# Kernel optimization log

Measured on AMD Instinct MI355X. Metric: run time of the kernel, lower is better.

## Reference

```python
import jax, jax.numpy as jnp
import numpy as np

FEAT_DIM = 2048
HIDDEN = 1024
ATTN_DIM = 512
BATCH = 128
NPOS = 196


def setup_inputs() -> dict:
    key = jax.random.key(0)
    ks = jax.random.split(key, 8)
    # Linear layers use kaiming-uniform-ish init; plain scaled normal is fine for a numeric baseline.
    def lin(k, fan_in, fan_out):
        k1, k2 = jax.random.split(k)
        bound = 1.0 / np.sqrt(fan_in)
        W = jax.random.uniform(k1, (fan_out, fan_in), jnp.float32, -bound, bound)
        b = jax.random.uniform(k2, (fan_out,), jnp.float32, -bound, bound)
        return W, b
    We, be = lin(ks[0], FEAT_DIM, ATTN_DIM)
    Wd, bd = lin(ks[1], HIDDEN, ATTN_DIM)
    Wf, bf = lin(ks[2], ATTN_DIM, 1)
    encoder_out = jax.random.normal(ks[3], (BATCH, NPOS, FEAT_DIM), jnp.float32)
    hidden = jax.random.normal(ks[4], (BATCH, HIDDEN), jnp.float32)
    return {
        "encoder_out": encoder_out,
        "hidden": hidden,
        "We": We, "be": be,
        "Wd": Wd, "bd": bd,
        "Wf": Wf, "bf": bf,
    }


def reference(encoder_out, hidden, We, be, Wd, bd, Wf, bf):
    # enc: [B, P, A]; dec: [B, 1, A]
    enc = jnp.einsum('bpf,af->bpa', encoder_out, We) + be
    dec = (jnp.einsum('bh,ah->ba', hidden, Wd) + bd)[:, None, :]
    scores = jnp.tanh(enc + dec)
    # full_attn: [A] -> scalar per position; Wf has shape [1, A]
    scores = jnp.einsum('bpa,a->bp', scores, Wf[0]) + bf[0]
    alpha = jax.nn.softmax(scores, axis=1)  # [B, P]
    context = jnp.einsum('bpf,bp->bf', encoder_out, alpha)  # [B, F]
    return context, alpha
```

## Files before the change

### kernel.cpp

```cpp
#include <hip/hip_runtime.h>
#include <hip/hip_bf16.h>

typedef __bf16 bf16x8 __attribute__((ext_vector_type(8)));
typedef __bf16 bf16x4 __attribute__((ext_vector_type(4)));
typedef float f32x4 __attribute__((ext_vector_type(4)));

#define FEAT 2048
#define HID  1024
#define AD   512
#define NB   128
#define NP   196
#define MROWS (NB * NP)
#define BM 128
#define BN 128
#define BK 64
#define NSTEP (FEAT / BK)
#define NBLK (MROWS / BM * 4)

__global__ __launch_bounds__(256) void pack_we_k(const float* __restrict__ We,
                                                 __bf16* __restrict__ Bp) {
    int t = blockIdx.x * 256 + threadIdx.x;
    int a  = t >> 8;
    int f0 = (t & 255) << 3;
    const float4* src = reinterpret_cast<const float4*>(We + ((size_t)a << 11) + f0);
    float4 x0 = src[0], x1 = src[1];
    int nt = a >> 4, r = a & 15;
    int kt = f0 >> 5, g = (f0 >> 3) & 3;
    size_t off = (((size_t)(kt * 32 + nt) * 64) + (r + (g << 4))) << 3;
    union { __bf16 h[8]; bf16x8 v; } u;
    u.h[0] = (__bf16)x0.x; u.h[1] = (__bf16)x0.y; u.h[2] = (__bf16)x0.z; u.h[3] = (__bf16)x0.w;
    u.h[4] = (__bf16)x1.x; u.h[5] = (__bf16)x1.y; u.h[6] = (__bf16)x1.z; u.h[7] = (__bf16)x1.w;
    *reinterpret_cast<bf16x8*>(Bp + off) = u.v;
}

__global__ __launch_bounds__(256) void dec_k(const float* __restrict__ hidden,
                                             const float* __restrict__ Wd,
                                             const float* __restrict__ bd,
                                             const float* __restrict__ be,
                                             float* __restrict__ decb) {
    __shared__ float w[8][1028];
    const int tid = threadIdx.x;
    const int n0 = blockIdx.x << 3;
    const float4* wsrc = reinterpret_cast<const float4*>(Wd + ((size_t)n0 << 10));
    #pragma unroll
    for (int i = 0; i < 8; ++i)
        *reinterpret_cast<float4*>(&w[i][tid << 2]) = wsrc[(i << 8) + tid];
    __syncthreads();
    const int nl = tid & 7, b0 = tid >> 3;
    float acc[4] = {0.f, 0.f, 0.f, 0.f};
    const float4* wp = reinterpret_cast<const float4*>(&w[nl][0]);
    #pragma unroll 2
    for (int k4 = 0; k4 < 256; ++k4) {
        float4 wv = wp[k4];
        #pragma unroll
        for (int i = 0; i < 4; ++i) {
            const float4 h = reinterpret_cast<const float4*>(
                hidden + ((size_t)(b0 + (i << 5)) << 10))[k4];
            acc[i] = fmaf(wv.x, h.x, acc[i]);
            acc[i] = fmaf(wv.y, h.y, acc[i]);
            acc[i] = fmaf(wv.z, h.z, acc[i]);
            acc[i] = fmaf(wv.w, h.w, acc[i]);
        }
    }
    const float bias = bd[n0 + nl] + be[n0 + nl];
    #pragma unroll
    for (int i = 0; i < 4; ++i)
        decb[(size_t)(b0 + (i << 5)) * AD + n0 + nl] = acc[i] + bias;
}

__global__ __launch_bounds__(256, 3) void enc_score_k(
        const float* __restrict__ X, const __bf16* __restrict__ Bp,
        const float* __restrict__ decb, const float* __restrict__ Wf,
        float* __restrict__ spart) {
    __shared__ char Asm[2][BM * BK * 2];
    __shared__ float swave[2][BM];
    const int tid  = threadIdx.x;
    const int wave = tid >> 6, lane = tid & 63;
    const int lr = lane & 15, lg = lane >> 4;
    const int wm = wave >> 1, wn = wave & 1;
    const int vbid = (blockIdx.x & 7) * 98 + (blockIdx.x >> 3);
    const int rt = vbid >> 2, nq = vbid & 3;
    const int row0 = rt * BM;
    const int ncol0 = nq * BN + wn * 64;

    f32x4 acc[4][4];
    #pragma unroll
    for (int mt = 0; mt < 4; ++mt) {
        #pragma unroll
        for (int j = 0; j < 4; ++j) {
            const int row = wm * 64 + mt * 16 + lg * 4 + j;
            const int b = (unsigned)(row0 + row) / 196u;
            const float* dp = decb + (size_t)b * AD + ncol0 + lr;
            #pragma unroll
            for (int nt = 0; nt < 4; ++nt) acc[mt][nt][j] = dp[nt * 16];
        }
    }

    const int srow = tid >> 4;
    const int schk = tid & 15;
    const float* gA = X + (size_t)(row0 + srow) * FEAT + schk * 4;
    const int rswz = (lr & 7) << 4;
    const __bf16* Bq = Bp + ((size_t)(nq * 8 + wn * 4) << 9) + (lane << 3);

    float4 rA[8];
    #pragma unroll
    for (int i = 0; i < 8; ++i)
        rA[i] = *reinterpret_cast<const float4*>(gA + (size_t)(i * 16) * FEAT);
    #pragma unroll
    for (int i = 0; i < 8; ++i) {
        const int r = srow + 16 * i;
        union { __bf16 h[4]; bf16x4 v; } p;
        p.h[0] = (__bf16)rA[i].x; p.h[1] = (__bf16)rA[i].y;
        p.h[2] = (__bf16)rA[i].z; p.h[3] = (__bf16)rA[i].w;
        *reinterpret_cast<bf16x4*>(Asm[0] + r * 128 + ((schk * 8) ^ ((r & 7) << 4))) = p.v;
    }
    __syncthreads();

    int cur = 0;
    for (int t = 0; t < NSTEP; ++t) {
        bf16x8 bfr[8];
        {
            const __bf16* bs = Bq + (size_t)t * 32768;
            #pragma unroll
            for (int kt2 = 0; kt2 < 2; ++kt2)
                #pragma unroll
                for (int j = 0; j < 4; ++j)
                    bfr[kt2 * 4 + j] = *reinterpret_cast<const bf16x8*>(
                        bs + kt2 * 16384 + j * 512);
        }
        __builtin_amdgcn_sched_barrier(0);
        if (t + 1 < NSTEP) {
            const float* g = gA + (size_t)(t + 1) * BK;
            #pragma unroll
            for (int i = 0; i < 8; ++i)
                rA[i] = *reinterpret_cast<const float4*>(g + (size_t)(i * 16) * FEAT);
        }
        __builtin_amdgcn_sched_barrier(0);
        #pragma unroll
        for (int kt2 = 0; kt2 < 2; ++kt2) {
            #pragma unroll
            for (int mt = 0; mt < 4; ++mt) {
                const int R = wm * 64 + mt * 16 + lr;
                bf16x8 a = *reinterpret_cast<const bf16x8*>(
                    Asm[cur] + R * 128 + ((kt2 * 64 + lg * 16) ^ rswz));
                acc[mt][0] = __builtin_amdgcn_mfma_f32_16x16x32_bf16(a, bfr[kt2*4+0], acc[mt][0], 0, 0, 0);
                acc[mt][1] = __builtin_amdgcn_mfma_f32_16x16x32_bf16(a, bfr[kt2*4+1], acc[mt][1], 0, 0, 0);
                acc[mt][2] = __builtin_amdgcn_mfma_f32_16x16x32_bf16(a, bfr[kt2*4+2], acc[mt][2], 0, 0, 0);
                acc[mt][3] = __builtin_amdgcn_mfma_f32_16x16x32_bf16(a, bfr[kt2*4+3], acc[mt][3], 0, 0, 0);
            }
        }
        if (t + 1 < NSTEP) {
            #pragma unroll
            for (int i = 0; i < 8; ++i) {
                const int r = srow + 16 * i;
                union { __bf16 h[4]; bf16x4 v; } p;
                p.h[0] = (__bf16)rA[i].x; p.h[1] = (__bf16)rA[i].y;
                p.h[2] = (__bf16)rA[i].z; p.h[3] = (__bf16)rA[i].w;
                *reinterpret_cast<bf16x4*>(
                    Asm[cur ^ 1] + r * 128 + ((schk * 8) ^ ((r & 7) << 4))) = p.v;
            }
        }
        __syncthreads();
        cur ^= 1;
    }

    float wf[4];
    #pragma unroll
    for (int nt = 0; nt < 4; ++nt) wf[nt] = Wf[ncol0 + nt * 16 + lr];
    #pragma unroll
    for (int mt = 0; mt < 4; ++mt) {
        #pragma unroll
        for (int j = 0; j < 4; ++j) {
            float s = 0.f;
            #pragma unroll
            for (int nt = 0; nt < 4; ++nt) {
                float x = acc[mt][nt][j];
                float e = __expf(2.0f * x);
                float t = 1.0f - 2.0f / (e + 1.0f);
                s = fmaf(t, wf[nt], s);
            }
            s += __shfl_xor(s, 1); s += __shfl_xor(s, 2);
            s += __shfl_xor(s, 4); s += __shfl_xor(s, 8);
            if (lr == 0) swave[wn][wm * 64 + mt * 16 + lg * 4 + j] = s;
        }
    }
    __syncthreads();
    if (tid < BM)
        spart[(size_t)nq * MROWS + row0 + tid] = swave[0][tid] + swave[1][tid];
}

__global__ __launch_bounds__(64) void softmax_k(const float* __restrict__ spart,
                                                float* __restrict__ alpha) {
    const int b = blockIdx.x, lane = threadIdx.x;
    float v[4], e[4];
    float m = -3.0e38f;
    #pragma unroll
    for (int i = 0; i < 4; ++i) {
        int p = i * 64 + lane;
        if (p < NP) {
            int idx = b * NP + p;
            v[i] = spart[idx] + spart[MROWS + idx] + spart[2 * MROWS + idx]
                 + spart[3 * MROWS + idx];
        } else v[i] = -3.0e38f;
        m = fmaxf(m, v[i]);
    }
    #pragma unroll
    for (int o = 1; o < 64; o <<= 1) m = fmaxf(m, __shfl_xor(m, o));
    float s = 0.f;
    #pragma unroll
    for (int i = 0; i < 4; ++i) {
        int p = i * 64 + lane;
        e[i] = (p < NP) ? __expf(v[i] - m) : 0.f;
        s += e[i];
    }
    #pragma unroll
    for (int o = 1; o < 64; o <<= 1) s += __shfl_xor(s, o);
    const float inv = 1.0f / s;
    #pragma unroll
    for (int i = 0; i < 4; ++i) {
        int p = i * 64 + lane;
        if (p < NP) alpha[b * NP + p] = e[i] * inv;
    }
}

__global__ __launch_bounds__(128) void context_k(const float* __restrict__ X,
                                                 const float* __restrict__ alpha,
                                                 float* __restrict__ ctx) {
    __shared__ float al[NP];
    const int bid = blockIdx.x;
    const int b = 127 - (bid >> 2);
    const int chunk = bid & 3;
    const int tid = threadIdx.x;
    for (int i = tid; i < NP; i += 128) al[i] = alpha[b * NP + i];
    __syncthreads();
    const float4* Xp = reinterpret_cast<const float4*>(X + (size_t)b * NP * FEAT)
                       + chunk * 128 + tid;
    float4 a0 = {0,0,0,0}, a1 = {0,0,0,0};
    #pragma unroll 4
    for (int p = 0; p < NP; p += 2) {
        const float w0 = al[p], w1 = al[p + 1];
        const float4 x0 = Xp[(size_t)p * 512];
        const float4 x1 = Xp[(size_t)(p + 1) * 512];
        a0.x = fmaf(w0, x0.x, a0.x); a0.y = fmaf(w0, x0.y, a0.y);
        a0.z = fmaf(w0, x0.z, a0.z); a0.w = fmaf(w0, x0.w, a0.w);
        a1.x = fmaf(w1, x1.x, a1.x); a1.y = fmaf(w1, x1.y, a1.y);
        a1.z = fmaf(w1, x1.z, a1.z); a1.w = fmaf(w1, x1.w, a1.w);
    }
    float4 rr; rr.x = a0.x + a1.x; rr.y = a0.y + a1.y; rr.z = a0.z + a1.z; rr.w = a0.w + a1.w;
    *reinterpret_cast<float4*>(ctx + (size_t)b * FEAT + chunk * 512 + tid * 4) = rr;
}

extern "C" void kernel_launch(void* const* d_in, const int* in_sizes, int n_in,
                              void* d_out, int out_size, void* d_ws, size_t ws_size,
                              hipStream_t stream) {
    const float* enc    = (const float*)d_in[0];
    const float* hidden = (const float*)d_in[1];
    const float* We     = (const float*)d_in[2];
    const float* be     = (const float*)d_in[3];
    const float* Wd     = (const float*)d_in[4];
    const float* bd     = (const float*)d_in[5];
    const float* Wf     = (const float*)d_in[6];

    float* out   = (float*)d_out;
    float* ctx   = out;
    float* alpha = out + NB * FEAT;

    char* ws = (char*)d_ws;
    __bf16* Bp    = (__bf16*)ws;
    float*  decb  = (float*)(ws + (2u << 20));
    float*  spart = (float*)(ws + (2u << 20) + (256u << 10));

    pack_we_k  <<<dim3(512), dim3(256), 0, stream>>>(We, Bp);
    dec_k      <<<dim3(64),  dim3(256), 0, stream>>>(hidden, Wd, bd, be, decb);
    enc_score_k<<<dim3(NBLK), dim3(256), 0, stream>>>(enc, Bp, decb, Wf, spart);
    softmax_k  <<<dim3(NB),  dim3(64),  0, stream>>>(spart, alpha);
    context_k  <<<dim3(512), dim3(128), 0, stream>>>(enc, alpha, ctx);
}
```

Baseline: 174.1 us.

## Deepen A/B prefetch pipeline with double register sets and manual barriers

Restructures the GEMM main loop into a two-step unrolled pipeline with two register sets for both A (fp32 global loads) and B fragments. Loads of A now run two K-steps ahead and B one step ahead, with explicit lgkmcnt waits and raw s_barrier in place of __syncthreads. The aim is to hide global-load latency behind MFMA work. Occupancy hint drops from 3 to 2 blocks per CU to make room for the extra registers, which may reduce latency hiding across waves.

Measured after the change: 175.7 us. No clear change (+0.9%).

```diff
diff --git a/kernel.cpp b/kernel.cpp
--- a/kernel.cpp
+++ b/kernel.cpp
@@ -68,11 +68,55 @@
         decb[(size_t)(b0 + (i << 5)) * AD + n0 + nl] = acc[i] + bias;
 }
 
-__global__ __launch_bounds__(256, 3) void enc_score_k(
+__device__ __forceinline__ void load_a(const float* g, float4 r[8]) {
+    #pragma unroll
+    for (int i = 0; i < 8; ++i)
+        r[i] = *reinterpret_cast<const float4*>(g + (size_t)(i * 16) * FEAT);
+}
+
+__device__ __forceinline__ void write_a(char* base, int srow, int schk, const float4 r[8]) {
+    #pragma unroll
+    for (int i = 0; i < 8; ++i) {
+        const int rr = srow + 16 * i;
+        union { __bf16 h[4]; bf16x4 v; } p;
+        p.h[0] = (__bf16)r[i].x; p.h[1] = (__bf16)r[i].y;
+        p.h[2] = (__bf16)r[i].z; p.h[3] = (__bf16)r[i].w;
+        *reinterpret_cast<bf16x4*>(base + rr * 128 + ((schk * 8) ^ ((rr & 7) << 4))) = p.v;
+    }
+}
+
+__device__ __forceinline__ void load_b(const __bf16* bs, bf16x8 f[8]) {
+    #pragma unroll
+    for (int kt2 = 0; kt2 < 2; ++kt2)
+        #pragma unroll
+        for (int j = 0; j < 4; ++j)
+            f[kt2 * 4 + j] = *reinterpret_cast<const bf16x8*>(bs + kt2 * 16384 + j * 512);
+}
+
+__device__ __forceinline__ void mfma_step(const char* buf, const bf16x8 f[8],
+                                          int wm, int lr, int lg, int rswz,
+                                          f32x4 acc[4][4]) {
+    #pragma unroll
+    for (int kt2 = 0; kt2 < 2; ++kt2) {
+        #pragma unroll
+        for (int mt = 0; mt < 4; ++mt) {
+            const int R = wm * 64 + mt * 16 + lr;
+            bf16x8 a = *reinterpret_cast<const bf16x8*>(
+                buf + R * 128 + ((kt2 * 64 + lg * 16) ^ rswz));
+            acc[mt][0] = __builtin_amdgcn_mfma_f32_16x16x32_bf16(a, f[kt2*4+0], acc[mt][0], 0, 0, 0);
+            acc[mt][1] = __builtin_amdgcn_mfma_f32_16x16x32_bf16(a, f[kt2*4+1], acc[mt][1], 0, 0, 0);
+            acc[mt][2] = __builtin_amdgcn_mfma_f32_16x16x32_bf16(a, f[kt2*4+2], acc[mt][2], 0, 0, 0);
+            acc[mt][3] = __builtin_amdgcn_mfma_f32_16x16x32_bf16(a, f[kt2*4+3], acc[mt][3], 0, 0, 0);
+        }
+    }
+}
+
+__global__ __launch_bounds__(256, 2) void enc_score_k(
         const float* __restrict__ X, const __bf16* __restrict__ Bp,
         const float* __restrict__ decb, const float* __restrict__ Wf,
         float* __restrict__ spart) {
-    __shared__ char Asm[2][BM * BK * 2];
+    __shared__ char Asm0[BM * BK * 2];
+    __shared__ char Asm1[BM * BK * 2];
     __shared__ float swave[2][BM];
     const int tid  = threadIdx.x;
     const int wave = tid >> 6, lane = tid & 63;
@@ -102,66 +146,39 @@
     const int rswz = (lr & 7) << 4;
     const __bf16* Bq = Bp + ((size_t)(nq * 8 + wn * 4) << 9) + (lane << 3);
 
-    float4 rA[8];
-    #pragma unroll
-    for (int i = 0; i < 8; ++i)
-        rA[i] = *reinterpret_cast<const float4*>(gA + (size_t)(i * 16) * FEAT);
-    #pragma unroll
-    for (int i = 0; i < 8; ++i) {
-        const int r = srow + 16 * i;
-        union { __bf16 h[4]; bf16x4 v; } p;
-        p.h[0] = (__bf16)rA[i].x; p.h[1] = (__bf16)rA[i].y;
-        p.h[2] = (__bf16)rA[i].z; p.h[3] = (__bf16)rA[i].w;
-        *reinterpret_cast<bf16x4*>(Asm[0] + r * 128 + ((schk * 8) ^ ((r & 7) << 4))) = p.v;
-    }
-    __syncthreads();
-
-    int cur = 0;
-    for (int t = 0; t < NSTEP; ++t) {
-        bf16x8 bfr[8];
-        {
-            const __bf16* bs = Bq + (size_t)t * 32768;
-            #pragma unroll
-            for (int kt2 = 0; kt2 < 2; ++kt2)
-                #pragma unroll
-                for (int j = 0; j < 4; ++j)
-                    bfr[kt2 * 4 + j] = *reinterpret_cast<const bf16x8*>(
-                        bs + kt2 * 16384 + j * 512);
-        }
-        __builtin_amdgcn_sched_barrier(0);
-        if (t + 1 < NSTEP) {
-            const float* g = gA + (size_t)(t + 1) * BK;
-            #pragma unroll
-            for (int i = 0; i < 8; ++i)
-                rA[i] = *reinterpret_cast<const float4*>(g + (size_t)(i * 16) * FEAT);
-        }
-        __builtin_amdgcn_sched_barrier(0);
-        #pragma unroll
-        for (int kt2 = 0; kt2 < 2; ++kt2) {
-            #pragma unroll
-            for (int mt = 0; mt < 4; ++mt) {
-                const int R = wm * 64 + mt * 16 + lr;
-                bf16x8 a = *reinterpret_cast<const bf16x8*>(
-                    Asm[cur] + R * 128 + ((kt2 * 64 + lg * 16) ^ rswz));
-                acc[mt][0] = __builtin_amdgcn_mfma_f32_16x16x32_bf16(a, bfr[kt2*4+0], acc[mt][0], 0, 0, 0);
-                acc[mt][1] = __builtin_amdgcn_mfma_f32_16x16x32_bf16(a, bfr[kt2*4+1], acc[mt][1], 0, 0, 0);
-                acc[mt][2] = __builtin_amdgcn_mfma_f32_16x16x32_bf16(a, bfr[kt2*4+2], acc[mt][2], 0, 0, 0);
-                acc[mt][3] = __builtin_amdgcn_mfma_f32_16x16x32_bf16(a, bfr[kt2*4+3], acc[mt][3], 0, 0, 0);
-            }
-        }
-        if (t + 1 < NSTEP) {
-            #pragma unroll
-            for (int i = 0; i < 8; ++i) {
-                const int r = srow + 16 * i;
-                union { __bf16 h[4]; bf16x4 v; } p;
-                p.h[0] = (__bf16)rA[i].x; p.h[1] = (__bf16)rA[i].y;
-                p.h[2] = (__bf16)rA[i].z; p.h[3] = (__bf16)rA[i].w;
-                *reinterpret_cast<bf16x4*>(
-                    Asm[cur ^ 1] + r * 128 + ((schk * 8) ^ ((r & 7) << 4))) = p.v;
-            }
-        }
-        __syncthreads();
-        cur ^= 1;
+    float4 rAa[8], rAb[8];
+    bf16x8 bfrA[8], bfrB[8];
+
+    load_a(gA, rAa);
+    load_a(gA + BK, rAb);
+    load_b(Bq, bfrA);
+    write_a(Asm0, srow, schk, rAa);
+    asm volatile("s_waitcnt lgkmcnt(0)" ::: "memory");
+    __builtin_amdgcn_sched_barrier(0);
+    __builtin_amdgcn_s_barrier();
+
+    #pragma unroll 1
+    for (int t2 = 0; t2 < NSTEP; t2 += 2) {
+        load_b(Bq + (size_t)(t2 + 1) * 32768, bfrB);
+        if (t2 + 2 < NSTEP) load_a(gA + (size_t)(t2 + 2) * BK, rAa);
+        __builtin_amdgcn_sched_barrier(0);
+        mfma_step(Asm0, bfrA, wm, lr, lg, rswz, acc);
+        __builtin_amdgcn_sched_barrier(0);
+        write_a(Asm1, srow, schk, rAb);
+        asm volatile("s_waitcnt lgkmcnt(0)" ::: "memory");
+        __builtin_amdgcn_sched_barrier(0);
+        __builtin_amdgcn_s_barrier();
+        if (t2 + 2 < NSTEP) load_b(Bq + (size_t)(t2 + 2) * 32768, bfrA);
+        if (t2 + 3 < NSTEP) load_a(gA + (size_t)(t2 + 3) * BK, rAb);
+        __builtin_amdgcn_sched_barrier(0);
+        mfma_step(Asm1, bfrB, wm, lr, lg, rswz, acc);
+        if (t2 + 2 < NSTEP) {
+            __builtin_amdgcn_sched_barrier(0);
+            write_a(Asm0, srow, schk, rAa);
+            asm volatile("s_waitcnt lgkmcnt(0)" ::: "memory");
+            __builtin_amdgcn_sched_barrier(0);
+            __builtin_amdgcn_s_barrier();
+        }
     }
 
     float wf[4];
```
